# Kernel optimization log

Measured on AMD Instinct MI355X. Metric: run time of the kernel, lower is better.

Reference implementation:

```python
import jax, jax.numpy as jnp
import numpy as np

SCALE = 8.0  # sqrt(d_k), d_k = 64


def setup_inputs() -> dict:
    key = jax.random.key(0)
    kq, kk, kv = jax.random.split(key, 3)
    B, S, D = 16, 2048, 64
    q = jax.random.normal(kq, (B, S, D), dtype=jnp.float32)
    k = jax.random.normal(kk, (B, S, D), dtype=jnp.float32)
    v = jax.random.normal(kv, (B, S, D), dtype=jnp.float32)
    # causal mask: True = masked (future positions), broadcast to batch
    causal = jnp.triu(jnp.ones((S, S), dtype=jnp.bool_), k=1)
    mask = jnp.broadcast_to(causal, (B, S, S))
    return {"q": q, "k": k, "v": v, "mask": mask}


def reference(q, k, v, mask):
    # u = (q @ k^T) / scale  -> [B, S, S]
    u = jnp.einsum("bqd,bkd->bqk", q, k) / SCALE
    u = jnp.where(mask, -jnp.inf, u)
    attn = jax.nn.softmax(u, axis=2)
    output = jnp.einsum("bqk,bkd->bqd", attn, v)
    return (attn, output)
```

## Files before the change

kernel.cpp:

```cpp
#include <hip/hip_runtime.h>
#include <hip/hip_bf16.h>

typedef __attribute__((ext_vector_type(4))) float  f32x4;
typedef __attribute__((ext_vector_type(8))) __bf16 bf16x8;
typedef __attribute__((ext_vector_type(4))) __bf16 bf16x4;

#define S_DIM 2048
#define D_DIM 64
#define A2    0.180336880f
#define TPITCH 68

__device__ __forceinline__ int swz(int r, int c) {
    return r * 64 + (c ^ ((r & 7) << 3));
}

__device__ __forceinline__ void loadK4(const float* Kb, int kt, int tid, f32x4 kr[4]) {
    #pragma unroll
    for (int i = 0; i < 4; ++i)
        kr[i] = *(const f32x4*)(Kb + (size_t)(kt * 64 + (tid >> 4) + i * 16) * D_DIM
                                + (tid & 15) * 4);
}
__device__ __forceinline__ void writeK4(__bf16* buf, int tid, const f32x4 kr[4]) {
    #pragma unroll
    for (int i = 0; i < 4; ++i) {
        bf16x4 h;
        h[0] = (__bf16)kr[i][0]; h[1] = (__bf16)kr[i][1];
        h[2] = (__bf16)kr[i][2]; h[3] = (__bf16)kr[i][3];
        *(bf16x4*)&buf[swz((tid >> 4) + i * 16, (tid & 15) * 4)] = h;
    }
}
__device__ __forceinline__ void loadQfrag(const float* Qb, int w, int c0, int jb, bf16x8 qf[2]) {
    const float* qp = Qb + (w * 16 + c0) * D_DIM + jb * 8;
    #pragma unroll
    for (int h = 0; h < 2; ++h) {
        f32x4 x0 = *(const f32x4*)(qp + h * 32);
        f32x4 x1 = *(const f32x4*)(qp + h * 32 + 4);
        bf16x8 f;
        f[0] = (__bf16)x0[0]; f[1] = (__bf16)x0[1];
        f[2] = (__bf16)x0[2]; f[3] = (__bf16)x0[3];
        f[4] = (__bf16)x1[0]; f[5] = (__bf16)x1[1];
        f[6] = (__bf16)x1[2]; f[7] = (__bf16)x1[3];
        qf[h] = f;
    }
}
__device__ __forceinline__ void mfmaS(const __bf16* bufK, const bf16x8 qf[2],
                                      int c0, int jb, f32x4 sacc[4]) {
    #pragma unroll
    for (int nt = 0; nt < 4; ++nt) sacc[nt] = (f32x4){0.f, 0.f, 0.f, 0.f};
    #pragma unroll
    for (int kk = 0; kk < 2; ++kk) {
        #pragma unroll
        for (int nt = 0; nt < 4; ++nt) {
            bf16x8 kb = *(bf16x8*)&bufK[swz(nt * 16 + c0, kk * 32 + jb * 8)];
            sacc[nt] = __builtin_amdgcn_mfma_f32_16x16x32_bf16(qf[kk], kb, sacc[nt], 0, 0, 0);
        }
    }
}

__global__ __launch_bounds__(256) void pvpart_kernel(
    const float* __restrict__ Q, const float* __restrict__ K,
    const float* __restrict__ V, __bf16* __restrict__ obase,
    float* __restrict__ lbase)
{
    __shared__ __attribute__((aligned(16))) __bf16 ldsK[2][64 * 64];
    __shared__ __attribute__((aligned(16))) __bf16 ldsV[2][64 * 64];
    __shared__ __attribute__((aligned(16))) __bf16 ldsP[64 * 64];

    const int tid = threadIdx.x, lane = tid & 63, w = tid >> 6;
    const int c0 = lane & 15, jb = lane >> 4;

    const int sid = ((blockIdx.x & 7) << 8) | (blockIdx.x >> 3);
    const int b = sid >> 7, qt = (sid >> 2) & 31, ck = sid & 3;
    if (ck * 8 > qt) return;
    const int k0 = ck * 8, kend = min(k0 + 8, qt + 1);
    const int q0 = qt * 64;

    const float* Kb = K + (size_t)b * S_DIM * D_DIM;
    const float* Vb = V + (size_t)b * S_DIM * D_DIM;

    bf16x8 qf[2];
    loadQfrag(Q + ((size_t)b * S_DIM + q0) * D_DIM, w, c0, jb, qf);

    float l2[4] = {0.f, 0.f, 0.f, 0.f};
    f32x4 oacc[4];
    #pragma unroll
    for (int nt = 0; nt < 4; ++nt) oacc[nt] = (f32x4){0.f, 0.f, 0.f, 0.f};

    f32x4 kr[4]; float vv[16];
    loadK4(Kb, k0, tid, kr);
    #pragma unroll
    for (int i = 0; i < 16; ++i)
        vv[i] = Vb[(size_t)(k0 * 64 + w * 16 + i) * D_DIM + lane];
    writeK4(ldsK[0], tid, kr);
    {
        bf16x8 h0, h1;
        #pragma unroll
        for (int j = 0; j < 8; ++j) { h0[j] = (__bf16)vv[j]; h1[j] = (__bf16)vv[8 + j]; }
        *(bf16x8*)&ldsV[0][swz(lane, w * 16)]     = h0;
        *(bf16x8*)&ldsV[0][swz(lane, w * 16 + 8)] = h1;
    }
    __syncthreads();

    int cur = 0;
    for (int kt = k0; kt < kend; ++kt) {
        const bool nxt = (kt + 1 < kend);
        if (nxt) {
            loadK4(Kb, kt + 1, tid, kr);
            #pragma unroll
            for (int i = 0; i < 16; ++i)
                vv[i] = Vb[(size_t)((kt + 1) * 64 + w * 16 + i) * D_DIM + lane];
        }
        f32x4 sacc[4];
        mfmaS(ldsK[cur], qf, c0, jb, sacc);
        const bool diag = (kt == qt);
        #pragma unroll
        for (int nt = 0; nt < 4; ++nt) {
            #pragma unroll
            for (int reg = 0; reg < 4; ++reg) {
                const int qr = w * 16 + jb * 4 + reg;
                const int kc = nt * 16 + c0;
                float p = (diag && kc > qr) ? 0.0f : exp2f(sacc[nt][reg] * A2);
                ldsP[swz(qr, kc)] = (__bf16)p;
                l2[reg] += p;
            }
        }
        #pragma unroll
        for (int kk = 0; kk < 2; ++kk) {
            bf16x8 pa = *(bf16x8*)&ldsP[swz(w * 16 + c0, kk * 32 + jb * 8)];
            #pragma unroll
            for (int nt = 0; nt < 4; ++nt) {
                bf16x8 vb = *(bf16x8*)&ldsV[cur][swz(nt * 16 + c0, kk * 32 + jb * 8)];
                oacc[nt] = __builtin_amdgcn_mfma_f32_16x16x32_bf16(pa, vb, oacc[nt], 0, 0, 0);
            }
        }
        if (nxt) {
            writeK4(ldsK[cur ^ 1], tid, kr);
            bf16x8 h0, h1;
            #pragma unroll
            for (int j = 0; j < 8; ++j) { h0[j] = (__bf16)vv[j]; h1[j] = (__bf16)vv[8 + j]; }
            *(bf16x8*)&ldsV[cur ^ 1][swz(lane, w * 16)]     = h0;
            *(bf16x8*)&ldsV[cur ^ 1][swz(lane, w * 16 + 8)] = h1;
        }
        __syncthreads();
        cur ^= 1;
    }

    const size_t strip = (size_t)(b * 32 + qt) * 4 + ck;
    #pragma unroll
    for (int reg = 0; reg < 4; ++reg) {
        float l = l2[reg];
        #pragma unroll
        for (int off = 1; off < 16; off <<= 1) l += __shfl_xor(l, off);
        if (c0 == 0) lbase[strip * 64 + w * 16 + jb * 4 + reg] = l;
    }
    #pragma unroll
    for (int nt = 0; nt < 4; ++nt) {
        #pragma unroll
        for (int reg = 0; reg < 4; ++reg) {
            const int qr = w * 16 + jb * 4 + reg;
            obase[strip * 4096 + qr * 64 + nt * 16 + c0] = (__bf16)oacc[nt][reg];
        }
    }
}

__global__ __launch_bounds__(256) void merge_kernel(
    const __bf16* __restrict__ obase, const float* __restrict__ lbase,
    float* __restrict__ out, float* __restrict__ cef)
{
    const int b  = blockIdx.x >> 5, qt = blockIdx.x & 31;
    const int q0 = qt * 64;
    const int nch = (qt >> 3) + 1;
    const int tid = threadIdx.x;
    const int r = tid >> 2, g = tid & 3;

    float acc[16];
    #pragma unroll
    for (int j = 0; j < 16; ++j) acc[j] = 0.f;
    float lsum = 0.f;
    const size_t base_strip = (size_t)(b * 32 + qt) * 4;
    for (int cc = 0; cc < nch; ++cc) {
        const size_t strip = base_strip + cc;
        const __bf16* op = obase + strip * 4096 + r * 64 + g * 16;
        bf16x8 a0 = *(bf16x8*)op;
        bf16x8 a1 = *(bf16x8*)(op + 8);
        #pragma unroll
        for (int j = 0; j < 8; ++j) { acc[j] += (float)a0[j]; acc[8 + j] += (float)a1[j]; }
        lsum += lbase[strip * 64 + r];
    }
    const float inv = 1.0f / lsum;
    float* dst = out + ((size_t)b * S_DIM + q0 + r) * D_DIM + g * 16;
    #pragma unroll
    for (int v = 0; v < 4; ++v) {
        f32x4 o;
        o[0] = acc[v*4+0] * inv; o[1] = acc[v*4+1] * inv;
        o[2] = acc[v*4+2] * inv; o[3] = acc[v*4+3] * inv;
        *(f32x4*)(dst + v * 4) = o;
    }
    if (g == 0) cef[b * S_DIM + q0 + r] = -log2f(lsum);
}

__global__ __launch_bounds__(256) void attn_tile_kernel(
    const float* __restrict__ Q, const float* __restrict__ K,
    float* __restrict__ attn, const float* __restrict__ cef)
{
    __shared__ __attribute__((aligned(16))) __bf16 ldsK[64 * 64];
    __shared__ __attribute__((aligned(16))) float  ldsT[64 * TPITCH];

    const int tid = threadIdx.x, lane = tid & 63, w = tid >> 6;
    const int c0 = lane & 15, jb = lane >> 4;

    const int sid = ((blockIdx.x & 7) << 11) | (blockIdx.x >> 3);
    const int b = sid >> 10, qt = (sid >> 5) & 31, kt = sid & 31;

    float* tileP = attn + ((size_t)b * S_DIM + qt * 64) * S_DIM + kt * 64;

    if (kt > qt) {
        f32x4 z = {0.f, 0.f, 0.f, 0.f};
        #pragma unroll
        for (int i = 0; i < 4; ++i) {
            int r  = i * 16 + (tid >> 4);
            int c4 = (tid & 15) * 4;
            *(f32x4*)&tileP[(size_t)r * S_DIM + c4] = z;
        }
        return;
    }

    const float* Kb = K + ((size_t)b * S_DIM + kt * 64) * D_DIM;
    #pragma unroll
    for (int i = 0; i < 4; ++i) {
        int r  = (tid >> 4) + i * 16;
        int c4 = (tid & 15) * 4;
        f32x4 x = *(const f32x4*)(Kb + (size_t)r * D_DIM + c4);
        bf16x4 h;
        h[0] = (__bf16)x[0]; h[1] = (__bf16)x[1];
        h[2] = (__bf16)x[2]; h[3] = (__bf16)x[3];
        *(bf16x4*)&ldsK[swz(r, c4)] = h;
    }
    bf16x8 qf[2];
    loadQfrag(Q + ((size_t)b * S_DIM + qt * 64) * D_DIM, w, c0, jb, qf);
    float ce[4];
    #pragma unroll
    for (int reg = 0; reg < 4; ++reg)
        ce[reg] = cef[b * S_DIM + qt * 64 + w * 16 + jb * 4 + reg];
    __syncthreads();

    f32x4 sacc[4];
    mfmaS(ldsK, qf, c0, jb, sacc);

    const bool diag = (kt == qt);
    #pragma unroll
    for (int nt = 0; nt < 4; ++nt) {
        #pragma unroll
        for (int reg = 0; reg < 4; ++reg) {
            const int qr = w * 16 + jb * 4 + reg;
            const int kc = nt * 16 + c0;
            float p = (diag && kc > qr) ? 0.0f
                    : exp2f(fmaf(sacc[nt][reg], A2, ce[reg]));
            ldsT[qr * TPITCH + kc] = p;
        }
    }
    __syncthreads();
    #pragma unroll
    for (int i = 0; i < 4; ++i) {
        int r  = i * 16 + (tid >> 4);
        int c4 = (tid & 15) * 4;
        f32x4 x = *(f32x4*)&ldsT[r * TPITCH + c4];
        *(f32x4*)&tileP[(size_t)r * S_DIM + c4] = x;
    }
}

extern "C" void kernel_launch(void* const* d_in, const int* in_sizes, int n_in,
                              void* d_out, int out_size, void* d_ws, size_t ws_size,
                              hipStream_t stream) {
    const float* Q = (const float*)d_in[0];
    const float* K = (const float*)d_in[1];
    const float* V = (const float*)d_in[2];
    float* attn = (float*)d_out;
    float* out  = attn + (size_t)16 * S_DIM * S_DIM;

    __bf16* obase = (__bf16*)d_ws;
    float*  lbase = (float*)((char*)d_ws + (size_t)2048 * 4096 * 2);
    float*  cef   = lbase + 2048 * 64;

    pvpart_kernel   <<<dim3(2048),  dim3(256), 0, stream>>>(Q, K, V, obase, lbase);
    merge_kernel    <<<dim3(512),   dim3(256), 0, stream>>>(obase, lbase, out, cef);
    attn_tile_kernel<<<dim3(16384), dim3(256), 0, stream>>>(Q, K, attn, cef);
}
```

Measured before the change: 108.2 us.

## Split upper-triangle zeroing into its own kernel and launch only lower-triangle tiles

Moves the zero-fill of masked tiles above the diagonal into a separate wide-store kernel that clears each row panel in 256-column chunks. The attention-tile kernel now launches only the 528 lower-triangular tiles per batch and recovers (qt, kt) from a triangular index with sqrt plus correction loops. This removes the many tiny zero-only blocks and their scheduling cost. The LDS readback is remapped so each wave reads only rows it wrote itself, which lets the second barrier be dropped. The cost is an extra kernel launch and index math per block.

```diff
diff --git a/kernel.cpp b/kernel.cpp
--- a/kernel.cpp
+++ b/kernel.cpp
@@ -199,6 +199,26 @@
     if (g == 0) cef[b * S_DIM + q0 + r] = -log2f(lsum);
 }
 
+__global__ __launch_bounds__(256) void zero4_kernel(float* __restrict__ attn) {
+    const int cx = blockIdx.x, qt = blockIdx.y, b = blockIdx.z;
+    const int col0 = (qt + 1) * 64 + cx * 256;
+    if (col0 >= S_DIM) return;
+    const int tid = threadIdx.x;
+    float* panel = attn + ((size_t)b * S_DIM + qt * 64) * S_DIM;
+    const int c = col0 + (tid & 15) * 16;
+    f32x4 z = {0.f, 0.f, 0.f, 0.f};
+    #pragma unroll
+    for (int i = 0; i < 4; ++i) {
+        const int r = i * 16 + (tid >> 4);
+        float* rowp = panel + (size_t)r * S_DIM;
+        #pragma unroll
+        for (int v = 0; v < 4; ++v) {
+            const int col = c + v * 4;
+            if (col < S_DIM) *(f32x4*)&rowp[col] = z;
+        }
+    }
+}
+
 __global__ __launch_bounds__(256) void attn_tile_kernel(
     const float* __restrict__ Q, const float* __restrict__ K,
     float* __restrict__ attn, const float* __restrict__ cef)
@@ -209,21 +229,15 @@
     const int tid = threadIdx.x, lane = tid & 63, w = tid >> 6;
     const int c0 = lane & 15, jb = lane >> 4;
 
-    const int sid = ((blockIdx.x & 7) << 11) | (blockIdx.x >> 3);
-    const int b = sid >> 10, qt = (sid >> 5) & 31, kt = sid & 31;
+    const int bx = blockIdx.x;
+    const int t  = (bx & 7) * 66 + (bx >> 3);
+    int qt = (int)((sqrtf(8.0f * t + 1.0f) - 1.0f) * 0.5f);
+    while ((qt + 1) * (qt + 2) / 2 <= t) ++qt;
+    while (qt * (qt + 1) / 2 > t) --qt;
+    const int kt = t - qt * (qt + 1) / 2;
+    const int b  = blockIdx.y;
 
     float* tileP = attn + ((size_t)b * S_DIM + qt * 64) * S_DIM + kt * 64;
-
-    if (kt > qt) {
-        f32x4 z = {0.f, 0.f, 0.f, 0.f};
-        #pragma unroll
-        for (int i = 0; i < 4; ++i) {
-            int r  = i * 16 + (tid >> 4);
-            int c4 = (tid & 15) * 4;
-            *(f32x4*)&tileP[(size_t)r * S_DIM + c4] = z;
-        }
-        return;
-    }
 
     const float* Kb = K + ((size_t)b * S_DIM + kt * 64) * D_DIM;
     #pragma unroll
@@ -259,11 +273,10 @@
             ldsT[qr * TPITCH + kc] = p;
         }
     }
-    __syncthreads();
     #pragma unroll
     for (int i = 0; i < 4; ++i) {
-        int r  = i * 16 + (tid >> 4);
-        int c4 = (tid & 15) * 4;
+        const int r  = w * 16 + i * 4 + jb;
+        const int c4 = c0 * 4;
         f32x4 x = *(f32x4*)&ldsT[r * TPITCH + c4];
         *(f32x4*)&tileP[(size_t)r * S_DIM + c4] = x;
     }
@@ -282,7 +295,8 @@
     float*  lbase = (float*)((char*)d_ws + (size_t)2048 * 4096 * 2);
     float*  cef   = lbase + 2048 * 64;
 
-    pvpart_kernel   <<<dim3(2048),  dim3(256), 0, stream>>>(Q, K, V, obase, lbase);
-    merge_kernel    <<<dim3(512),   dim3(256), 0, stream>>>(obase, lbase, out, cef);
-    attn_tile_kernel<<<dim3(16384), dim3(256), 0, stream>>>(Q, K, attn, cef);
-}
+    pvpart_kernel   <<<dim3(2048),       dim3(256), 0, stream>>>(Q, K, V, obase, lbase);
+    merge_kernel    <<<dim3(512),        dim3(256), 0, stream>>>(obase, lbase, out, cef);
+    zero4_kernel    <<<dim3(8, 32, 16),  dim3(256), 0, stream>>>(attn);
+    attn_tile_kernel<<<dim3(528, 16),    dim3(256), 0, stream>>>(Q, K, attn, cef);
+}
```

Result: slower. 172.0 us (+58.9%).

## Compute attention probabilities in 64x256 panels per block instead of 64x64 tiles

Applied to the files above, without the earlier changes.

Each block of the attention-matrix writer now covers four consecutive key tiles (a 64x256 panel), so the Q fragment and row constants are loaded once per four tiles. There are a quarter as many blocks, and each thread stores 64-byte contiguous row segments. The LDS staging buffer now holds probabilities in bf16 rather than fp32 to fit the wider panel, which rounds the written attention values to bf16 precision before they are widened back to fp32.

```diff
diff --git a/kernel.cpp b/kernel.cpp
--- a/kernel.cpp
+++ b/kernel.cpp
@@ -8,7 +8,7 @@
 #define S_DIM 2048
 #define D_DIM 64
 #define A2    0.180336880f
-#define TPITCH 68
+#define PPITCH 264
 
 __device__ __forceinline__ int swz(int r, int c) {
     return r * 64 + (c ^ ((r & 7) << 3));
@@ -199,73 +199,96 @@
     if (g == 0) cef[b * S_DIM + q0 + r] = -log2f(lsum);
 }
 
-__global__ __launch_bounds__(256) void attn_tile_kernel(
+__global__ __launch_bounds__(256) void attn_panel_kernel(
     const float* __restrict__ Q, const float* __restrict__ K,
     float* __restrict__ attn, const float* __restrict__ cef)
 {
-    __shared__ __attribute__((aligned(16))) __bf16 ldsK[64 * 64];
-    __shared__ __attribute__((aligned(16))) float  ldsT[64 * TPITCH];
+    __shared__ __attribute__((aligned(16))) __bf16 ldsK[4][64 * 64];
+    __shared__ __attribute__((aligned(16))) __bf16 ldsP[64 * PPITCH];
 
     const int tid = threadIdx.x, lane = tid & 63, w = tid >> 6;
     const int c0 = lane & 15, jb = lane >> 4;
 
-    const int sid = ((blockIdx.x & 7) << 11) | (blockIdx.x >> 3);
-    const int b = sid >> 10, qt = (sid >> 5) & 31, kt = sid & 31;
-
-    float* tileP = attn + ((size_t)b * S_DIM + qt * 64) * S_DIM + kt * 64;
-
-    if (kt > qt) {
+    const int sid = ((blockIdx.x & 7) << 9) | (blockIdx.x >> 3);
+    const int b = sid >> 8, qt = (sid >> 3) & 31, px = sid & 7;
+    const int q0 = qt * 64;
+    const int ktmin = px * 4;
+
+    float* panel = attn + ((size_t)b * S_DIM + q0) * S_DIM + px * 256;
+
+    if (ktmin > qt) {
         f32x4 z = {0.f, 0.f, 0.f, 0.f};
         #pragma unroll
         for (int i = 0; i < 4; ++i) {
-            int r  = i * 16 + (tid >> 4);
-            int c4 = (tid & 15) * 4;
-            *(f32x4*)&tileP[(size_t)r * S_DIM + c4] = z;
+            const int r = i * 16 + (tid >> 4);
+            float* rowp = panel + (size_t)r * S_DIM + (tid & 15) * 16;
+            #pragma unroll
+            for (int v = 0; v < 4; ++v)
+                *(f32x4*)&rowp[v * 4] = z;
         }
         return;
     }
 
-    const float* Kb = K + ((size_t)b * S_DIM + kt * 64) * D_DIM;
+    const float* Kb = K + (size_t)b * S_DIM * D_DIM;
+    #pragma unroll
+    for (int tt = 0; tt < 4; ++tt) {
+        if (ktmin + tt <= qt) {
+            f32x4 kr[4];
+            loadK4(Kb, ktmin + tt, tid, kr);
+            writeK4(ldsK[tt], tid, kr);
+        }
+    }
+    bf16x8 qf[2];
+    loadQfrag(Q + ((size_t)b * S_DIM + q0) * D_DIM, w, c0, jb, qf);
+    float ce[4];
+    #pragma unroll
+    for (int reg = 0; reg < 4; ++reg)
+        ce[reg] = cef[b * S_DIM + q0 + w * 16 + jb * 4 + reg];
+    __syncthreads();
+
+    #pragma unroll
+    for (int tt = 0; tt < 4; ++tt) {
+        const int kt = ktmin + tt;
+        if (kt > qt) continue;
+        f32x4 sacc[4];
+        mfmaS(ldsK[tt], qf, c0, jb, sacc);
+        const bool diag = (kt == qt);
+        #pragma unroll
+        for (int nt = 0; nt < 4; ++nt) {
+            #pragma unroll
+            for (int reg = 0; reg < 4; ++reg) {
+                const int qr = w * 16 + jb * 4 + reg;
+                const int kc = nt * 16 + c0;
+                float p = (diag && kc > qr) ? 0.0f
+                        : exp2f(fmaf(sacc[nt][reg], A2, ce[reg]));
+                ldsP[qr * PPITCH + tt * 64 + kc] = (__bf16)p;
+            }
+        }
+    }
+    __syncthreads();
+
     #pragma unroll
     for (int i = 0; i < 4; ++i) {
-        int r  = (tid >> 4) + i * 16;
-        int c4 = (tid & 15) * 4;
-        f32x4 x = *(const f32x4*)(Kb + (size_t)r * D_DIM + c4);
-        bf16x4 h;
-        h[0] = (__bf16)x[0]; h[1] = (__bf16)x[1];
-        h[2] = (__bf16)x[2]; h[3] = (__bf16)x[3];
-        *(bf16x4*)&ldsK[swz(r, c4)] = h;
-    }
-    bf16x8 qf[2];
-    loadQfrag(Q + ((size_t)b * S_DIM + qt * 64) * D_DIM, w, c0, jb, qf);
-    float ce[4];
-    #pragma unroll
-    for (int reg = 0; reg < 4; ++reg)
-        ce[reg] = cef[b * S_DIM + qt * 64 + w * 16 + jb * 4 + reg];
-    __syncthreads();
-
-    f32x4 sacc[4];
-    mfmaS(ldsK, qf, c0, jb, sacc);
-
-    const bool diag = (kt == qt);
-    #pragma unroll
-    for (int nt = 0; nt < 4; ++nt) {
-        #pragma unroll
-        for (int reg = 0; reg < 4; ++reg) {
-            const int qr = w * 16 + jb * 4 + reg;
-            const int kc = nt * 16 + c0;
-            float p = (diag && kc > qr) ? 0.0f
-                    : exp2f(fmaf(sacc[nt][reg], A2, ce[reg]));
-            ldsT[qr * TPITCH + kc] = p;
-        }
-    }
-    __syncthreads();
-    #pragma unroll
-    for (int i = 0; i < 4; ++i) {
-        int r  = i * 16 + (tid >> 4);
-        int c4 = (tid & 15) * 4;
-        f32x4 x = *(f32x4*)&ldsT[r * TPITCH + c4];
-        *(f32x4*)&tileP[(size_t)r * S_DIM + c4] = x;
+        const int r     = i * 16 + (tid >> 4);
+        const int cbase = (tid & 15) * 16;
+        float* dst = panel + (size_t)r * S_DIM + cbase;
+        if (ktmin + (cbase >> 6) > qt) {
+            f32x4 z = {0.f, 0.f, 0.f, 0.f};
+            #pragma unroll
+            for (int v = 0; v < 4; ++v) *(f32x4*)&dst[v * 4] = z;
+        } else {
+            bf16x8 p0 = *(bf16x8*)&ldsP[r * PPITCH + cbase];
+            bf16x8 p1 = *(bf16x8*)&ldsP[r * PPITCH + cbase + 8];
+            f32x4 o0, o1, o2, o3;
+            o0[0] = (float)p0[0]; o0[1] = (float)p0[1]; o0[2] = (float)p0[2]; o0[3] = (float)p0[3];
+            o1[0] = (float)p0[4]; o1[1] = (float)p0[5]; o1[2] = (float)p0[6]; o1[3] = (float)p0[7];
+            o2[0] = (float)p1[0]; o2[1] = (float)p1[1]; o2[2] = (float)p1[2]; o2[3] = (float)p1[3];
+            o3[0] = (float)p1[4]; o3[1] = (float)p1[5]; o3[2] = (float)p1[6]; o3[3] = (float)p1[7];
+            *(f32x4*)&dst[0]  = o0;
+            *(f32x4*)&dst[4]  = o1;
+            *(f32x4*)&dst[8]  = o2;
+            *(f32x4*)&dst[12] = o3;
+        }
     }
 }
 
@@ -282,7 +305,7 @@
     float*  lbase = (float*)((char*)d_ws + (size_t)2048 * 4096 * 2);
     float*  cef   = lbase + 2048 * 64;
 
-    pvpart_kernel   <<<dim3(2048),  dim3(256), 0, stream>>>(Q, K, V, obase, lbase);
-    merge_kernel    <<<dim3(512),   dim3(256), 0, stream>>>(obase, lbase, out, cef);
-    attn_tile_kernel<<<dim3(16384), dim3(256), 0, stream>>>(Q, K, attn, cef);
-}
+    pvpart_kernel   <<<dim3(2048), dim3(256), 0, stream>>>(Q, K, V, obase, lbase);
+    merge_kernel    <<<dim3(512),  dim3(256), 0, stream>>>(obase, lbase, out, cef);
+    attn_panel_kernel<<<dim3(4096), dim3(256), 0, stream>>>(Q, K, attn, cef);
+}
```

New measurement: 155.9 us. 44.0% more time.

## Rebalance split-K chunks and batch four attention tiles per block

Applied to the files above, without the earlier changes.

The PV partial kernel now splits the key range into chunks of 4 tiles instead of 8 and launches twice as many blocks. It drops the double-buffered K/V prefetch in favour of single-buffered load-then-compute with a sync. The merge kernel is split per 16-row quad so more blocks run, and the attention-probability kernel handles four key tiles per block, reusing the Q fragments and row coefficients across them. The aim is better load balance and fewer redundant per-block setup costs, at the cost of lost load/compute overlap in the PV kernel and twice the partial-sum workspace traffic.

```diff
diff --git a/kernel.cpp b/kernel.cpp
--- a/kernel.cpp
+++ b/kernel.cpp
@@ -57,23 +57,24 @@
     }
 }
 
-__global__ __launch_bounds__(256) void pvpart_kernel(
+__global__ __launch_bounds__(256) void tile_pv4_kernel(
     const float* __restrict__ Q, const float* __restrict__ K,
     const float* __restrict__ V, __bf16* __restrict__ obase,
     float* __restrict__ lbase)
 {
-    __shared__ __attribute__((aligned(16))) __bf16 ldsK[2][64 * 64];
-    __shared__ __attribute__((aligned(16))) __bf16 ldsV[2][64 * 64];
+    __shared__ __attribute__((aligned(16))) __bf16 ldsK[64 * 64];
+    __shared__ __attribute__((aligned(16))) __bf16 ldsV[64 * 64];
     __shared__ __attribute__((aligned(16))) __bf16 ldsP[64 * 64];
 
     const int tid = threadIdx.x, lane = tid & 63, w = tid >> 6;
     const int c0 = lane & 15, jb = lane >> 4;
 
-    const int sid = ((blockIdx.x & 7) << 8) | (blockIdx.x >> 3);
-    const int b = sid >> 7, qt = (sid >> 2) & 31, ck = sid & 3;
-    if (ck * 8 > qt) return;
-    const int k0 = ck * 8, kend = min(k0 + 8, qt + 1);
+    const int sid = ((blockIdx.x & 7) << 9) | (blockIdx.x >> 3);
+    const int b = sid >> 8, qt = (sid >> 3) & 31, g = sid & 7;
+    if (g * 4 > qt) return;
+    const int k0 = g * 4, kend = min(k0 + 4, qt + 1);
     const int q0 = qt * 64;
+    const size_t slot = (size_t)sid;
 
     const float* Kb = K + (size_t)b * S_DIM * D_DIM;
     const float* Vb = V + (size_t)b * S_DIM * D_DIM;
@@ -86,32 +87,25 @@
     #pragma unroll
     for (int nt = 0; nt < 4; ++nt) oacc[nt] = (f32x4){0.f, 0.f, 0.f, 0.f};
 
-    f32x4 kr[4]; float vv[16];
-    loadK4(Kb, k0, tid, kr);
-    #pragma unroll
-    for (int i = 0; i < 16; ++i)
-        vv[i] = Vb[(size_t)(k0 * 64 + w * 16 + i) * D_DIM + lane];
-    writeK4(ldsK[0], tid, kr);
-    {
-        bf16x8 h0, h1;
-        #pragma unroll
-        for (int j = 0; j < 8; ++j) { h0[j] = (__bf16)vv[j]; h1[j] = (__bf16)vv[8 + j]; }
-        *(bf16x8*)&ldsV[0][swz(lane, w * 16)]     = h0;
-        *(bf16x8*)&ldsV[0][swz(lane, w * 16 + 8)] = h1;
-    }
-    __syncthreads();
-
-    int cur = 0;
     for (int kt = k0; kt < kend; ++kt) {
-        const bool nxt = (kt + 1 < kend);
-        if (nxt) {
-            loadK4(Kb, kt + 1, tid, kr);
+        f32x4 kr[4];
+        loadK4(Kb, kt, tid, kr);
+        writeK4(ldsK, tid, kr);
+        {
+            float vv[16];
             #pragma unroll
             for (int i = 0; i < 16; ++i)
-                vv[i] = Vb[(size_t)((kt + 1) * 64 + w * 16 + i) * D_DIM + lane];
-        }
+                vv[i] = Vb[(size_t)(kt * 64 + w * 16 + i) * D_DIM + lane];
+            bf16x8 h0, h1;
+            #pragma unroll
+            for (int j = 0; j < 8; ++j) { h0[j] = (__bf16)vv[j]; h1[j] = (__bf16)vv[8 + j]; }
+            *(bf16x8*)&ldsV[swz(lane, w * 16)]     = h0;
+            *(bf16x8*)&ldsV[swz(lane, w * 16 + 8)] = h1;
+        }
+        __syncthreads();
+
         f32x4 sacc[4];
-        mfmaS(ldsK[cur], qf, c0, jb, sacc);
+        mfmaS(ldsK, qf, c0, jb, sacc);
         const bool diag = (kt == qt);
         #pragma unroll
         for (int nt = 0; nt < 4; ++nt) {
@@ -129,77 +123,56 @@
             bf16x8 pa = *(bf16x8*)&ldsP[swz(w * 16 + c0, kk * 32 + jb * 8)];
             #pragma unroll
             for (int nt = 0; nt < 4; ++nt) {
-                bf16x8 vb = *(bf16x8*)&ldsV[cur][swz(nt * 16 + c0, kk * 32 + jb * 8)];
+                bf16x8 vb = *(bf16x8*)&ldsV[swz(nt * 16 + c0, kk * 32 + jb * 8)];
                 oacc[nt] = __builtin_amdgcn_mfma_f32_16x16x32_bf16(pa, vb, oacc[nt], 0, 0, 0);
             }
         }
-        if (nxt) {
-            writeK4(ldsK[cur ^ 1], tid, kr);
-            bf16x8 h0, h1;
-            #pragma unroll
-            for (int j = 0; j < 8; ++j) { h0[j] = (__bf16)vv[j]; h1[j] = (__bf16)vv[8 + j]; }
-            *(bf16x8*)&ldsV[cur ^ 1][swz(lane, w * 16)]     = h0;
-            *(bf16x8*)&ldsV[cur ^ 1][swz(lane, w * 16 + 8)] = h1;
-        }
-        __syncthreads();
-        cur ^= 1;
-    }
-
-    const size_t strip = (size_t)(b * 32 + qt) * 4 + ck;
+        __syncthreads();
+    }
+
     #pragma unroll
     for (int reg = 0; reg < 4; ++reg) {
         float l = l2[reg];
         #pragma unroll
         for (int off = 1; off < 16; off <<= 1) l += __shfl_xor(l, off);
-        if (c0 == 0) lbase[strip * 64 + w * 16 + jb * 4 + reg] = l;
+        if (c0 == 0) lbase[slot * 64 + w * 16 + jb * 4 + reg] = l;
     }
     #pragma unroll
     for (int nt = 0; nt < 4; ++nt) {
         #pragma unroll
         for (int reg = 0; reg < 4; ++reg) {
             const int qr = w * 16 + jb * 4 + reg;
-            obase[strip * 4096 + qr * 64 + nt * 16 + c0] = (__bf16)oacc[nt][reg];
-        }
-    }
-}
-
-__global__ __launch_bounds__(256) void merge_kernel(
+            obase[slot * 4096 + qr * 64 + nt * 16 + c0] = (__bf16)oacc[nt][reg];
+        }
+    }
+}
+
+__global__ __launch_bounds__(256) void merge4_kernel(
     const __bf16* __restrict__ obase, const float* __restrict__ lbase,
     float* __restrict__ out, float* __restrict__ cef)
 {
-    const int b  = blockIdx.x >> 5, qt = blockIdx.x & 31;
-    const int q0 = qt * 64;
-    const int nch = (qt >> 3) + 1;
+    const int sid = ((blockIdx.x & 7) << 8) | (blockIdx.x >> 3);
+    const int b = sid >> 7, qt = (sid >> 2) & 31, quad = sid & 3;
     const int tid = threadIdx.x;
-    const int r = tid >> 2, g = tid & 3;
-
-    float acc[16];
-    #pragma unroll
-    for (int j = 0; j < 16; ++j) acc[j] = 0.f;
-    float lsum = 0.f;
-    const size_t base_strip = (size_t)(b * 32 + qt) * 4;
-    for (int cc = 0; cc < nch; ++cc) {
-        const size_t strip = base_strip + cc;
-        const __bf16* op = obase + strip * 4096 + r * 64 + g * 16;
-        bf16x8 a0 = *(bf16x8*)op;
-        bf16x8 a1 = *(bf16x8*)(op + 8);
-        #pragma unroll
-        for (int j = 0; j < 8; ++j) { acc[j] += (float)a0[j]; acc[8 + j] += (float)a1[j]; }
-        lsum += lbase[strip * 64 + r];
+    const int r  = quad * 16 + (tid >> 4);
+    const int c4 = (tid & 15) * 4;
+    const int ng = (qt >> 2) + 1;
+    const size_t base = (size_t)(b * 32 + qt) * 8;
+
+    float a0 = 0.f, a1 = 0.f, a2 = 0.f, a3 = 0.f, lsum = 0.f;
+    for (int g = 0; g < ng; ++g) {
+        const __bf16* op = obase + (base + g) * 4096 + r * 64 + c4;
+        bf16x4 a = *(const bf16x4*)op;
+        a0 += (float)a[0]; a1 += (float)a[1]; a2 += (float)a[2]; a3 += (float)a[3];
+        lsum += lbase[(base + g) * 64 + r];
     }
     const float inv = 1.0f / lsum;
-    float* dst = out + ((size_t)b * S_DIM + q0 + r) * D_DIM + g * 16;
-    #pragma unroll
-    for (int v = 0; v < 4; ++v) {
-        f32x4 o;
-        o[0] = acc[v*4+0] * inv; o[1] = acc[v*4+1] * inv;
-        o[2] = acc[v*4+2] * inv; o[3] = acc[v*4+3] * inv;
-        *(f32x4*)(dst + v * 4) = o;
-    }
-    if (g == 0) cef[b * S_DIM + q0 + r] = -log2f(lsum);
-}
-
-__global__ __launch_bounds__(256) void attn_tile_kernel(
+    f32x4 o = {a0 * inv, a1 * inv, a2 * inv, a3 * inv};
+    *(f32x4*)&out[((size_t)b * S_DIM + qt * 64 + r) * D_DIM + c4] = o;
+    if ((tid & 15) == 0) cef[b * S_DIM + qt * 64 + r] = -log2f(lsum);
+}
+
+__global__ __launch_bounds__(256) void attn_tile4_kernel(
     const float* __restrict__ Q, const float* __restrict__ K,
     float* __restrict__ attn, const float* __restrict__ cef)
 {
@@ -209,63 +182,76 @@
     const int tid = threadIdx.x, lane = tid & 63, w = tid >> 6;
     const int c0 = lane & 15, jb = lane >> 4;
 
-    const int sid = ((blockIdx.x & 7) << 11) | (blockIdx.x >> 3);
-    const int b = sid >> 10, qt = (sid >> 5) & 31, kt = sid & 31;
-
-    float* tileP = attn + ((size_t)b * S_DIM + qt * 64) * S_DIM + kt * 64;
-
-    if (kt > qt) {
+    const int sid = ((blockIdx.x & 7) << 9) | (blockIdx.x >> 3);
+    const int b = sid >> 8, qt = (sid >> 3) & 31, px = sid & 7;
+    const int q0 = qt * 64;
+    const int ktbase = px * 4;
+
+    float* rowbase = attn + ((size_t)b * S_DIM + q0) * S_DIM;
+
+    if (ktbase > qt) {
         f32x4 z = {0.f, 0.f, 0.f, 0.f};
+        #pragma unroll
+        for (int tt = 0; tt < 4; ++tt) {
+            float* tileP = rowbase + (ktbase + tt) * 64;
+            #pragma unroll
+            for (int i = 0; i < 4; ++i) {
+                int r  = i * 16 + (tid >> 4);
+                int c4 = (tid & 15) * 4;
+                *(f32x4*)&tileP[(size_t)r * S_DIM + c4] = z;
+            }
+        }
+        return;
+    }
+
+    const float* Kb = K + (size_t)b * S_DIM * D_DIM;
+    bf16x8 qf[2];
+    loadQfrag(Q + ((size_t)b * S_DIM + q0) * D_DIM, w, c0, jb, qf);
+    float ce[4];
+    #pragma unroll
+    for (int reg = 0; reg < 4; ++reg)
+        ce[reg] = cef[b * S_DIM + q0 + w * 16 + jb * 4 + reg];
+
+    for (int tt = 0; tt < 4; ++tt) {
+        const int kt = ktbase + tt;
+        float* tileP = rowbase + kt * 64;
+        if (kt > qt) {
+            f32x4 z = {0.f, 0.f, 0.f, 0.f};
+            #pragma unroll
+            for (int i = 0; i < 4; ++i) {
+                int r  = i * 16 + (tid >> 4);
+                int c4 = (tid & 15) * 4;
+                *(f32x4*)&tileP[(size_t)r * S_DIM + c4] = z;
+            }
+            continue;
+        }
+        f32x4 kr[4];
+        loadK4(Kb, kt, tid, kr);
+        writeK4(ldsK, tid, kr);
+        __syncthreads();
+
+        f32x4 sacc[4];
+        mfmaS(ldsK, qf, c0, jb, sacc);
+        const bool diag = (kt == qt);
+        #pragma unroll
+        for (int nt = 0; nt < 4; ++nt) {
+            #pragma unroll
+            for (int reg = 0; reg < 4; ++reg) {
+                const int qr = w * 16 + jb * 4 + reg;
+                const int kc = nt * 16 + c0;
+                float p = (diag && kc > qr) ? 0.0f
+                        : exp2f(fmaf(sacc[nt][reg], A2, ce[reg]));
+                ldsT[qr * TPITCH + kc] = p;
+            }
+        }
+        __syncthreads();
         #pragma unroll
         for (int i = 0; i < 4; ++i) {
             int r  = i * 16 + (tid >> 4);
             int c4 = (tid & 15) * 4;
-            *(f32x4*)&tileP[(size_t)r * S_DIM + c4] = z;
-        }
-        return;
-    }
-
-    const float* Kb = K + ((size_t)b * S_DIM + kt * 64) * D_DIM;
-    #pragma unroll
-    for (int i = 0; i < 4; ++i) {
-        int r  = (tid >> 4) + i * 16;
-        int c4 = (tid & 15) * 4;
-        f32x4 x = *(const f32x4*)(Kb + (size_t)r * D_DIM + c4);
-        bf16x4 h;
-        h[0] = (__bf16)x[0]; h[1] = (__bf16)x[1];
-        h[2] = (__bf16)x[2]; h[3] = (__bf16)x[3];
-        *(bf16x4*)&ldsK[swz(r, c4)] = h;
-    }
-    bf16x8 qf[2];
-    loadQfrag(Q + ((size_t)b * S_DIM + qt * 64) * D_DIM, w, c0, jb, qf);
-    float ce[4];
-    #pragma unroll
-    for (int reg = 0; reg < 4; ++reg)
-        ce[reg] = cef[b * S_DIM + qt * 64 + w * 16 + jb * 4 + reg];
-    __syncthreads();
-
-    f32x4 sacc[4];
-    mfmaS(ldsK, qf, c0, jb, sacc);
-
-    const bool diag = (kt == qt);
-    #pragma unroll
-    for (int nt = 0; nt < 4; ++nt) {
-        #pragma unroll
-        for (int reg = 0; reg < 4; ++reg) {
-            const int qr = w * 16 + jb * 4 + reg;
-            const int kc = nt * 16 + c0;
-            float p = (diag && kc > qr) ? 0.0f
-                    : exp2f(fmaf(sacc[nt][reg], A2, ce[reg]));
-            ldsT[qr * TPITCH + kc] = p;
-        }
-    }
-    __syncthreads();
-    #pragma unroll
-    for (int i = 0; i < 4; ++i) {
-        int r  = i * 16 + (tid >> 4);
-        int c4 = (tid & 15) * 4;
-        f32x4 x = *(f32x4*)&ldsT[r * TPITCH + c4];
-        *(f32x4*)&tileP[(size_t)r * S_DIM + c4] = x;
+            f32x4 x = *(f32x4*)&ldsT[r * TPITCH + c4];
+            *(f32x4*)&tileP[(size_t)r * S_DIM + c4] = x;
+        }
     }
 }
 
@@ -279,10 +265,10 @@
     float* out  = attn + (size_t)16 * S_DIM * S_DIM;
 
     __bf16* obase = (__bf16*)d_ws;
-    float*  lbase = (float*)((char*)d_ws + (size_t)2048 * 4096 * 2);
-    float*  cef   = lbase + 2048 * 64;
-
-    pvpart_kernel   <<<dim3(2048),  dim3(256), 0, stream>>>(Q, K, V, obase, lbase);
-    merge_kernel    <<<dim3(512),   dim3(256), 0, stream>>>(obase, lbase, out, cef);
-    attn_tile_kernel<<<dim3(16384), dim3(256), 0, stream>>>(Q, K, attn, cef);
-}
+    float*  lbase = (float*)((char*)d_ws + (size_t)4096 * 4096 * 2);
+    float*  cef   = lbase + (size_t)4096 * 64;
+
+    tile_pv4_kernel <<<dim3(4096), dim3(256), 0, stream>>>(Q, K, V, obase, lbase);
+    merge4_kernel   <<<dim3(2048), dim3(256), 0, stream>>>(obase, lbase, out, cef);
+    attn_tile4_kernel<<<dim3(4096), dim3(256), 0, stream>>>(Q, K, attn, cef);
+}
```

Measured after the change: 95.84 us (median of 2 runs). 1.13x faster.
